# Performance work log

Hardware: AMD Instinct MI355X
Metric: run time of the kernel (lower is better)

## Reference

```python
import jax, jax.numpy as jnp
import numpy as np

D_IN, H1, H2, B, K = 128, 128, 64, 262144, 4

def _mk(key, shape):
    return jax.random.normal(key, shape, dtype=jnp.float32) * 0.05

def setup_inputs() -> dict:
    key = jax.random.key(0)
    ks = jax.random.split(key, 40)
    inp = {
        'x': jax.random.normal(ks[0], (B, 96), dtype=jnp.float32),
        'u': jax.random.normal(ks[1], (B, 32), dtype=jnp.float32),
        'mix_factor': jax.random.uniform(ks[2], (1,), dtype=jnp.float32),
        'teacher_P': jax.random.uniform(ks[3], (K,), dtype=jnp.float32),
    }
    # main critic params (torch Linear: W [out,in], b [out])
    dims = [(H1, D_IN), (H1, H1), (H2, H1), (1, H2)] * 2  # l1..l4, l5..l8
    for i, (o, ii) in enumerate(dims):
        inp[f'W{i+1}'] = _mk(ks[4 + 2 * i], (o, ii))
        inp[f'b{i+1}'] = _mk(ks[5 + 2 * i], (o,))
    # stacked teacher params (K teachers), only l1,l2,l3,l5,l6,l7 are used
    tdims = {'1': (H1, D_IN), '2': (H1, H1), '3': (H2, H1), '5': (H1, D_IN), '6': (H1, H1), '7': (H2, H1)}
    j = 20
    for name, (o, ii) in tdims.items():
        inp[f'tW{name}'] = _mk(ks[j], (K, o, ii)); j += 1
        inp[f'tb{name}'] = _mk(ks[j], (K, o)); j += 1
    return inp

def reference(x, u, mix_factor, teacher_P, W1, b1, W2, b2, W3, b3, W4, b4, W5, b5, W6, b6, W7, b7, W8, b8, tW1, tb1, tW2, tb2, tW3, tb3, tW5, tb5, tW6, tb6, tW7, tb7):
    m = mix_factor  # [1], broadcasts
    P = teacher_P   # [K]
    xu = jnp.concatenate([x, u], axis=1)  # [B, 128]

    lin = lambda h, W, b: h @ W.T + b
    # teacher linear on shared input [B,I] -> [K,B,O]
    tlin0 = lambda h, W, b: jnp.einsum('bi,koi->kbo', h, W) + b[:, None, :]
    # teacher linear on per-teacher streams [K,B,I] -> [K,B,O]
    tlin = lambda h, W, b: jnp.einsum('kbi,koi->kbo', h, W) + b[:, None, :]
    mixsum = lambda ht: jnp.einsum('kbo,k->bo', ht, P)

    def head(W_a, b_a, W_b, b_b, W_c, b_c, W_d, b_d, tWa, tba, tWb, tbb, tWc, tbc):
        ht = tlin0(xu, tWa, tba)                                   # [K,B,128]
        h = jax.nn.relu(lin(xu, W_a, b_a) * (1 - m) + mixsum(ht) * m)
        ht = jax.nn.relu(ht)
        ht2 = tlin(ht, tWb, tbb)
        h = jax.nn.relu(lin(h, W_b, b_b) * (1 - m) + mixsum(ht2) * m)
        ht2 = jax.nn.relu(ht2)
        ht3 = tlin(ht2, tWc, tbc)
        h = jax.nn.relu(lin(h, W_c, b_c) * (1 - m) + mixsum(ht3) * m)
        return lin(h, W_d, b_d)                                    # [B,1]

    x1 = head(W1, b1, W2, b2, W3, b3, W4, b4, tW1, tb1, tW2, tb2, tW3, tb3)
    x2 = head(W5, b5, W6, b6, W7, b7, W8, b8, tW5, tb5, tW6, tb6, tW7, tb7)
    return (x1, x2)
```

## Files before the change

kernel.cpp:

```cpp
#include <hip/hip_runtime.h>
#include <hip/hip_bf16.h>
#include <stdint.h>

#define B_TOTAL 262144
#define TB 64
#define RECORD 2560
#define LDS_BYTES 163840
#define HEAD_W 204800

typedef short v8s __attribute__((ext_vector_type(8)));
typedef float v4f __attribute__((ext_vector_type(4)));

union Frag { uint4 q; uint32_t d[4]; v8s v; };

__device__ __forceinline__ uint32_t pack2(float a, float b) {
    union { __hip_bfloat162 h; uint32_t u; } p;
    p.h = __float22bfloat162_rn(make_float2(a, b));
    return p.u;
}


struct KParams {
    const float* x; const float* u; const float* mix; const float* P;
    const float* mb[6];
    const float* tb[6];
    const float* Wout[2];
    const float* bout[2];
    const unsigned short* wbf;
    float* out;
};

struct PrepParams { const float* src[12]; unsigned short* dst; };

__global__ __launch_bounds__(256) void prep_kernel(PrepParams pp) {
    const int ends[12] = {16384,81920,98304,163840,172032,204800,
                          221184,286720,303104,368640,376832,409600};
    int gi = (blockIdx.x * 256 + threadIdx.x) * 4;
    if (gi >= 409600) return;
    int s = 0;
    #pragma unroll
    for (int i = 0; i < 12; ++i) { if (gi >= ends[i]) s = i + 1; }
    int base = (s == 0) ? 0 : ends[s - 1];
    const float4 f = *(const float4*)(pp.src[s] + (gi - base));
    *(uint2*)(pp.dst + gi) = make_uint2(pack2(f.x, f.y), pack2(f.z, f.w));
}

__device__ __forceinline__ void stage_xu(char* lds, const float* x, const float* u,
                                         int rowBase, int tid)
{
    for (int G = tid; G < 1024; G += 512) {
        const int row = G >> 4;
        const int gg  = G & 15;
        const int grow = rowBase + row;
        float4 fa, fb;
        if (gg < 12) {
            const float* s2 = x + grow * 96 + gg * 8;
            fa = *(const float4*)s2; fb = *(const float4*)(s2 + 4);
        } else {
            const float* s2 = u + grow * 32 + (gg - 12) * 8;
            fa = *(const float4*)s2; fb = *(const float4*)(s2 + 4);
        }
        *(uint4*)(lds + row * RECORD + ((gg ^ (row & 15)) << 4)) =
            make_uint4(pack2(fa.x, fa.y), pack2(fa.z, fa.w),
                       pack2(fb.x, fb.y), pack2(fb.z, fb.w));
    }
}

struct WPre { Frag w[20]; float4 mB; float4 tB[4]; };

template<int N>
__device__ __forceinline__ WPre preload(const unsigned short* W,
        const float* mbias, const float* tbias, int lane, int wave)
{
    WPre r;
    const int l15  = lane & 15;
    const int quad = lane >> 4;
    const int colBase = (N == 64) ? ((wave >> 1) << 4) : (wave << 4);
    const unsigned short* wRow = W + (colBase + l15) * 128 + quad * 8;
    #pragma unroll
    for (int s = 0; s < 5; ++s)
        #pragma unroll
        for (int ks = 0; ks < 4; ++ks)
            r.w[s * 4 + ks].q = *(const uint4*)(wRow + s * (N * 128) + ks * 32);
    const int obase = colBase + quad * 4;
    r.mB = *(const float4*)(mbias + obase);
    #pragma unroll
    for (int s = 0; s < 4; ++s)
        r.tB[s] = *(const float4*)(tbias + s * N + obase);
    return r;
}

template<bool SHARED_IN, int N, int INS, int OUTS>
__device__ __forceinline__ void compute(char* lds,
        const WPre& wp, float c0, const float* cP, int lane, int wave,
        const float* Wout, float* pgrid)
{
    constexpr bool FINAL = (N == 64);
    constexpr int NBT = FINAL ? 2 : 4;
    const int l15  = lane & 15;
    const int quad = lane >> 4;
    const int colBase = FINAL ? ((wave >> 1) << 4) : (wave << 4);
    const int btBase  = FINAL ? ((wave & 1) << 1) : 0;

    const uint32_t rb = (uint32_t)l15 * RECORD + ((uint32_t)l15 << 4);
    uint32_t rA[4];
    #pragma unroll
    for (int ks = 0; ks < 4; ++ks)
        rA[ks] = rb ^ (uint32_t)(((ks << 2) | quad) << 4);
    if constexpr (FINAL) {
        const uint32_t bo = (uint32_t)btBase * 40960u;
        #pragma unroll
        for (int ks = 0; ks < 4; ++ks) rA[ks] += bo;
    }
    uint32_t rB[4];
    if constexpr (!FINAL) {
        #pragma unroll
        for (int ks = 0; ks < 4; ++ks) rB[ks] = rA[ks] + 2u * 40960u;
    }

    v4f acc[5][NBT];
    #pragma unroll
    for (int bt = 0; bt < NBT; ++bt) {
        acc[0][bt] = (v4f){wp.mB.x, wp.mB.y, wp.mB.z, wp.mB.w};
        #pragma unroll
        for (int s = 0; s < 4; ++s)
            acc[s + 1][bt] = (v4f){wp.tB[s].x, wp.tB[s].y, wp.tB[s].z, wp.tB[s].w};
    }

    #pragma unroll
    for (int ks = 0; ks < 4; ++ks) {
        Frag xS[NBT];
        if constexpr (SHARED_IN) {
            #pragma unroll
            for (int bt = 0; bt < NBT; ++bt) {
                const uint32_t a = (bt < 2) ? (rA[ks] + (uint32_t)(bt * 40960 + INS * 256))
                                            : (rB[ks] + (uint32_t)((bt - 2) * 40960 + INS * 256));
                xS[bt].q = *(const uint4*)(lds + a);
            }
        }
        #pragma unroll
        for (int s = 0; s < 5; ++s) {
            Frag xF[NBT];
            if constexpr (!SHARED_IN) {
                #pragma unroll
                for (int bt = 0; bt < NBT; ++bt) {
                    const uint32_t a = (bt < 2) ? (rA[ks] + (uint32_t)(bt * 40960 + (INS + s) * 256))
                                                : (rB[ks] + (uint32_t)((bt - 2) * 40960 + (INS + s) * 256));
                    xF[bt].q = *(const uint4*)(lds + a);
                }
            }
            #pragma unroll
            for (int bt = 0; bt < NBT; ++bt)
                acc[s][bt] = __builtin_amdgcn_mfma_f32_16x16x32_bf16(
                    wp.w[s * 4 + ks].v, (SHARED_IN ? xS[bt].v : xF[bt].v),
                    acc[s][bt], 0, 0, 0);
        }
    }

    const int obase = colBase + (quad << 2);

    if constexpr (!FINAL) {
        const int ocg = (colBase >> 3) + (quad >> 1);
        const uint32_t w0 = (rb ^ ((uint32_t)ocg << 4)) + (uint32_t)((quad & 1) << 3);
        #pragma unroll
        for (int bt = 0; bt < 4; ++bt) {
            char* ab = lds + (w0 + (uint32_t)(bt * 40960));
            float vr[4];
            vr[0] = c0 * acc[0][bt][0];
            vr[1] = c0 * acc[0][bt][1];
            vr[2] = c0 * acc[0][bt][2];
            vr[3] = c0 * acc[0][bt][3];
            uint2 tw[4];
            #pragma unroll
            for (int s = 0; s < 4; ++s) {
                const float t0 = acc[s + 1][bt][0];
                const float t1 = acc[s + 1][bt][1];
                const float t2 = acc[s + 1][bt][2];
                const float t3 = acc[s + 1][bt][3];
                vr[0] = fmaf(cP[s], t0, vr[0]);
                vr[1] = fmaf(cP[s], t1, vr[1]);
                vr[2] = fmaf(cP[s], t2, vr[2]);
                vr[3] = fmaf(cP[s], t3, vr[3]);
                tw[s] = make_uint2(pack2(fmaxf(t0, 0.f), fmaxf(t1, 0.f)),
                                   pack2(fmaxf(t2, 0.f), fmaxf(t3, 0.f)));
            }
            *(uint2*)(ab + OUTS * 256) =
                make_uint2(pack2(fmaxf(vr[0], 0.f), fmaxf(vr[1], 0.f)),
                           pack2(fmaxf(vr[2], 0.f), fmaxf(vr[3], 0.f)));
            #pragma unroll
            for (int s = 0; s < 4; ++s)
                *(uint2*)(ab + (OUTS + 1 + s) * 256) = tw[s];
        }
    } else {
        const float4 wo = *(const float4*)(Wout + obase);
        float psum[NBT];
        #pragma unroll
        for (int j = 0; j < NBT; ++j) {
            float vr[4];
            vr[0] = c0 * acc[0][j][0];
            vr[1] = c0 * acc[0][j][1];
            vr[2] = c0 * acc[0][j][2];
            vr[3] = c0 * acc[0][j][3];
            #pragma unroll
            for (int s = 0; s < 4; ++s) {
                vr[0] = fmaf(cP[s], acc[s + 1][j][0], vr[0]);
                vr[1] = fmaf(cP[s], acc[s + 1][j][1], vr[1]);
                vr[2] = fmaf(cP[s], acc[s + 1][j][2], vr[2]);
                vr[3] = fmaf(cP[s], acc[s + 1][j][3], vr[3]);
            }
            float pp = fmaxf(vr[0], 0.f) * wo.x + fmaxf(vr[1], 0.f) * wo.y
                     + fmaxf(vr[2], 0.f) * wo.z + fmaxf(vr[3], 0.f) * wo.w;
            pp += __shfl_xor(pp, 16);
            pp += __shfl_xor(pp, 32);
            psum[j] = pp;
        }
        if (lane < 16) {
            #pragma unroll
            for (int j = 0; j < NBT; ++j)
                pgrid[(wave >> 1) * 64 + (btBase + j) * 16 + lane] = psum[j];
        }
    }
}

extern "C" __global__ __launch_bounds__(512, 2)
void critic_kernel(KParams p)
{
    extern __shared__ char lds[];
    const int tid  = threadIdx.x;
    const int lane = tid & 63;
    const int wave = tid >> 6;
    const int rowBase = blockIdx.x * TB;

    const float m  = p.mix[0];
    const float c0 = 1.f - m;
    float cP[4];
    #pragma unroll
    for (int k = 0; k < 4; ++k) cP[k] = m * p.P[k];

    stage_xu(lds, p.x, p.u, rowBase, tid);

    #pragma unroll 1
    for (int head = 0; head < 2; ++head) {
        const unsigned short* wb = p.wbf + head * HEAD_W;
        const int hb = head * 3;

        WPre w1 = preload<128>(wb, p.mb[hb + 0], p.tb[hb + 0], lane, wave);
        __syncthreads();
        compute<true, 128, 0, 5>(lds, w1, c0, cP, lane, wave, nullptr, nullptr);

        WPre w2 = preload<128>(wb + 81920, p.mb[hb + 1], p.tb[hb + 1], lane, wave);
        __syncthreads();
        compute<false, 128, 5, 0>(lds, w2, c0, cP, lane, wave, nullptr, nullptr);

        WPre w3 = preload<64>(wb + 163840, p.mb[hb + 2], p.tb[hb + 2], lane, wave);
        __syncthreads();
        compute<false, 64, 0, 0>(lds, w3, c0, cP, lane, wave,
                                 p.Wout[head], (float*)(lds + 1280));
        __syncthreads();

        if (tid < 64) {
            const float* pg = (const float*)(lds + 1280);
            p.out[head * B_TOTAL + rowBase + tid] =
                p.bout[head][0] + pg[tid] + pg[64 + tid] + pg[128 + tid] + pg[192 + tid];
        }
        if (head == 0) {
            stage_xu(lds, p.x, p.u, rowBase, tid);
        }
    }
}

extern "C" void kernel_launch(void* const* d_in, const int* in_sizes, int n_in,
                              void* d_out, int out_size, void* d_ws, size_t ws_size,
                              hipStream_t stream)
{
    (void)in_sizes; (void)n_in; (void)out_size; (void)ws_size;

    PrepParams pp;
    const int sidx[12] = {4, 20, 6, 22, 8, 24, 12, 26, 14, 28, 16, 30};
    for (int i = 0; i < 12; ++i) pp.src[i] = (const float*)d_in[sidx[i]];
    pp.dst = (unsigned short*)d_ws;

    KParams kp;
    kp.x = (const float*)d_in[0];  kp.u = (const float*)d_in[1];
    kp.mix = (const float*)d_in[2]; kp.P = (const float*)d_in[3];
    const int mbi[6] = {5, 7, 9, 13, 15, 17};
    const int tbi[6] = {21, 23, 25, 27, 29, 31};
    for (int i = 0; i < 6; ++i) {
        kp.mb[i] = (const float*)d_in[mbi[i]];
        kp.tb[i] = (const float*)d_in[tbi[i]];
    }
    kp.Wout[0] = (const float*)d_in[10]; kp.Wout[1] = (const float*)d_in[18];
    kp.bout[0] = (const float*)d_in[11]; kp.bout[1] = (const float*)d_in[19];
    kp.wbf = (const unsigned short*)d_ws;
    kp.out = (float*)d_out;

    (void)hipFuncSetAttribute((const void*)critic_kernel,
                              hipFuncAttributeMaxDynamicSharedMemorySize, LDS_BYTES);

    hipLaunchKernelGGL(prep_kernel, dim3(400), dim3(256), 0, stream, pp);
    hipLaunchKernelGGL(critic_kernel, dim3(B_TOTAL / TB), dim3(512), LDS_BYTES, stream, kp);
}
```

Baseline: 860.3 us.

## Halve batch tile to 32 rows with 4 waves each computing two column tiles

Shrinks the per-block batch tile from 64 to 32 rows and the block from 512 to 256 threads, halving LDS use so more blocks can be resident per CU. Each wave now covers two 16-column output tiles per layer, reloading weight fragments from global/L2 between them, and the batch tiles per wave drop from 4 to 2. It also raises wave priority around the MFMA loop with s_setprio. The cost is twice as many weight-fragment loads per row processed, and more blocks overall, each staging its own inputs.

```diff
diff --git a/kernel.cpp b/kernel.cpp
--- a/kernel.cpp
+++ b/kernel.cpp
@@ -3,9 +3,9 @@
 #include <stdint.h>
 
 #define B_TOTAL 262144
-#define TB 64
+#define TB 32
 #define RECORD 2560
-#define LDS_BYTES 163840
+#define LDS_BYTES 81920
 #define HEAD_W 204800
 
 typedef short v8s __attribute__((ext_vector_type(8)));
@@ -48,7 +48,7 @@
 __device__ __forceinline__ void stage_xu(char* lds, const float* x, const float* u,
                                          int rowBase, int tid)
 {
-    for (int G = tid; G < 1024; G += 512) {
+    for (int G = tid; G < 512; G += 256) {
         const int row = G >> 4;
         const int gg  = G & 15;
         const int grow = rowBase + row;
@@ -69,13 +69,12 @@
 struct WPre { Frag w[20]; float4 mB; float4 tB[4]; };
 
 template<int N>
-__device__ __forceinline__ WPre preload(const unsigned short* W,
-        const float* mbias, const float* tbias, int lane, int wave)
+__device__ __forceinline__ WPre preload(const unsigned short* W, int colBase,
+        const float* mbias, const float* tbias, int lane)
 {
     WPre r;
     const int l15  = lane & 15;
     const int quad = lane >> 4;
-    const int colBase = (N == 64) ? ((wave >> 1) << 4) : (wave << 4);
     const unsigned short* wRow = W + (colBase + l15) * 128 + quad * 8;
     #pragma unroll
     for (int s = 0; s < 5; ++s)
@@ -92,70 +91,55 @@
 
 template<bool SHARED_IN, int N, int INS, int OUTS>
 __device__ __forceinline__ void compute(char* lds,
-        const WPre& wp, float c0, const float* cP, int lane, int wave,
+        const WPre& wp, float c0, const float* cP, int lane, int colBase,
         const float* Wout, float* pgrid)
 {
     constexpr bool FINAL = (N == 64);
-    constexpr int NBT = FINAL ? 2 : 4;
     const int l15  = lane & 15;
     const int quad = lane >> 4;
-    const int colBase = FINAL ? ((wave >> 1) << 4) : (wave << 4);
-    const int btBase  = FINAL ? ((wave & 1) << 1) : 0;
 
     const uint32_t rb = (uint32_t)l15 * RECORD + ((uint32_t)l15 << 4);
     uint32_t rA[4];
     #pragma unroll
     for (int ks = 0; ks < 4; ++ks)
         rA[ks] = rb ^ (uint32_t)(((ks << 2) | quad) << 4);
-    if constexpr (FINAL) {
-        const uint32_t bo = (uint32_t)btBase * 40960u;
-        #pragma unroll
-        for (int ks = 0; ks < 4; ++ks) rA[ks] += bo;
-    }
-    uint32_t rB[4];
-    if constexpr (!FINAL) {
-        #pragma unroll
-        for (int ks = 0; ks < 4; ++ks) rB[ks] = rA[ks] + 2u * 40960u;
-    }
-
-    v4f acc[5][NBT];
-    #pragma unroll
-    for (int bt = 0; bt < NBT; ++bt) {
+
+    v4f acc[5][2];
+    #pragma unroll
+    for (int bt = 0; bt < 2; ++bt) {
         acc[0][bt] = (v4f){wp.mB.x, wp.mB.y, wp.mB.z, wp.mB.w};
         #pragma unroll
         for (int s = 0; s < 4; ++s)
             acc[s + 1][bt] = (v4f){wp.tB[s].x, wp.tB[s].y, wp.tB[s].z, wp.tB[s].w};
     }
 
+    __builtin_amdgcn_s_setprio(1);
     #pragma unroll
     for (int ks = 0; ks < 4; ++ks) {
-        Frag xS[NBT];
+        Frag xS[2];
         if constexpr (SHARED_IN) {
             #pragma unroll
-            for (int bt = 0; bt < NBT; ++bt) {
-                const uint32_t a = (bt < 2) ? (rA[ks] + (uint32_t)(bt * 40960 + INS * 256))
-                                            : (rB[ks] + (uint32_t)((bt - 2) * 40960 + INS * 256));
-                xS[bt].q = *(const uint4*)(lds + a);
-            }
+            for (int bt = 0; bt < 2; ++bt)
+                xS[bt].q = *(const uint4*)(lds + rA[ks]
+                            + (uint32_t)(bt * 40960 + INS * 256));
         }
         #pragma unroll
         for (int s = 0; s < 5; ++s) {
-            Frag xF[NBT];
+            Frag xF[2];
             if constexpr (!SHARED_IN) {
                 #pragma unroll
-                for (int bt = 0; bt < NBT; ++bt) {
-                    const uint32_t a = (bt < 2) ? (rA[ks] + (uint32_t)(bt * 40960 + (INS + s) * 256))
-                                                : (rB[ks] + (uint32_t)((bt - 2) * 40960 + (INS + s) * 256));
-                    xF[bt].q = *(const uint4*)(lds + a);
-                }
+                for (int bt = 0; bt < 2; ++bt)
+                    xF[bt].q = *(const uint4*)(lds + rA[ks]
+                                + (uint32_t)(bt * 40960 + (INS + s) * 256));
             }
             #pragma unroll
-            for (int bt = 0; bt < NBT; ++bt)
+            for (int bt = 0; bt < 2; ++bt)
                 acc[s][bt] = __builtin_amdgcn_mfma_f32_16x16x32_bf16(
                     wp.w[s * 4 + ks].v, (SHARED_IN ? xS[bt].v : xF[bt].v),
                     acc[s][bt], 0, 0, 0);
         }
     }
+    __builtin_amdgcn_s_setprio(0);
 
     const int obase = colBase + (quad << 2);
 
@@ -163,7 +147,7 @@
         const int ocg = (colBase >> 3) + (quad >> 1);
         const uint32_t w0 = (rb ^ ((uint32_t)ocg << 4)) + (uint32_t)((quad & 1) << 3);
         #pragma unroll
-        for (int bt = 0; bt < 4; ++bt) {
+        for (int bt = 0; bt < 2; ++bt) {
             char* ab = lds + (w0 + (uint32_t)(bt * 40960));
             float vr[4];
             vr[0] = c0 * acc[0][bt][0];
@@ -193,9 +177,10 @@
         }
     } else {
         const float4 wo = *(const float4*)(Wout + obase);
-        float psum[NBT];
-        #pragma unroll
-        for (int j = 0; j < NBT; ++j) {
+        const int cw = colBase >> 4;
+        float psum[2];
+        #pragma unroll
+        for (int j = 0; j < 2; ++j) {
             float vr[4];
             vr[0] = c0 * acc[0][j][0];
             vr[1] = c0 * acc[0][j][1];
@@ -216,13 +201,13 @@
         }
         if (lane < 16) {
             #pragma unroll
-            for (int j = 0; j < NBT; ++j)
-                pgrid[(wave >> 1) * 64 + (btBase + j) * 16 + lane] = psum[j];
-        }
-    }
-}
-
-extern "C" __global__ __launch_bounds__(512, 2)
+            for (int j = 0; j < 2; ++j)
+                pgrid[cw * 32 + j * 16 + lane] = psum[j];
+        }
+    }
+}
+
+extern "C" __global__ __launch_bounds__(256, 2)
 void critic_kernel(KParams p)
 {
     extern __shared__ char lds[];
@@ -230,6 +215,8 @@
     const int lane = tid & 63;
     const int wave = tid >> 6;
     const int rowBase = blockIdx.x * TB;
+    const int cb32 = wave << 5;
+    const int cb16 = wave << 4;
 
     const float m  = p.mix[0];
     const float c0 = 1.f - m;
@@ -244,24 +231,28 @@
         const unsigned short* wb = p.wbf + head * HEAD_W;
         const int hb = head * 3;
 
-        WPre w1 = preload<128>(wb, p.mb[hb + 0], p.tb[hb + 0], lane, wave);
-        __syncthreads();
-        compute<true, 128, 0, 5>(lds, w1, c0, cP, lane, wave, nullptr, nullptr);
-
-        WPre w2 = preload<128>(wb + 81920, p.mb[hb + 1], p.tb[hb + 1], lane, wave);
-        __syncthreads();
-        compute<false, 128, 5, 0>(lds, w2, c0, cP, lane, wave, nullptr, nullptr);
-
-        WPre w3 = preload<64>(wb + 163840, p.mb[hb + 2], p.tb[hb + 2], lane, wave);
-        __syncthreads();
-        compute<false, 64, 0, 0>(lds, w3, c0, cP, lane, wave,
+        WPre w = preload<128>(wb, cb32, p.mb[hb + 0], p.tb[hb + 0], lane);
+        __syncthreads();
+        compute<true, 128, 0, 5>(lds, w, c0, cP, lane, cb32, nullptr, nullptr);
+        w = preload<128>(wb, cb32 + 16, p.mb[hb + 0], p.tb[hb + 0], lane);
+        compute<true, 128, 0, 5>(lds, w, c0, cP, lane, cb32 + 16, nullptr, nullptr);
+
+        w = preload<128>(wb + 81920, cb32, p.mb[hb + 1], p.tb[hb + 1], lane);
+        __syncthreads();
+        compute<false, 128, 5, 0>(lds, w, c0, cP, lane, cb32, nullptr, nullptr);
+        w = preload<128>(wb + 81920, cb32 + 16, p.mb[hb + 1], p.tb[hb + 1], lane);
+        compute<false, 128, 5, 0>(lds, w, c0, cP, lane, cb32 + 16, nullptr, nullptr);
+
+        w = preload<64>(wb + 163840, cb16, p.mb[hb + 2], p.tb[hb + 2], lane);
+        __syncthreads();
+        compute<false, 64, 0, 0>(lds, w, c0, cP, lane, cb16,
                                  p.Wout[head], (float*)(lds + 1280));
         __syncthreads();
 
-        if (tid < 64) {
+        if (tid < 32) {
             const float* pg = (const float*)(lds + 1280);
             p.out[head * B_TOTAL + rowBase + tid] =
-                p.bout[head][0] + pg[tid] + pg[64 + tid] + pg[128 + tid] + pg[192 + tid];
+                p.bout[head][0] + pg[tid] + pg[32 + tid] + pg[64 + tid] + pg[96 + tid];
         }
         if (head == 0) {
             stage_xu(lds, p.x, p.u, rowBase, tid);
@@ -298,5 +289,5 @@
                               hipFuncAttributeMaxDynamicSharedMemorySize, LDS_BYTES);
 
     hipLaunchKernelGGL(prep_kernel, dim3(400), dim3(256), 0, stream, pp);
-    hipLaunchKernelGGL(critic_kernel, dim3(B_TOTAL / TB), dim3(512), LDS_BYTES, stream, kp);
-}
+    hipLaunchKernelGGL(critic_kernel, dim3(B_TOTAL / TB), dim3(256), LDS_BYTES, stream, kp);
+}
```

Result: slower. 1.063 ms (+23.6%).

## Double block to 1024 threads, splitting batch tiles across twice as many waves

Applied to the files above, without the earlier changes.

The critic kernel now launches 1024 threads per block instead of 512. Each wave handles half as many 16-row batch tiles: 2 instead of 4 in the 128-wide layers, and 1 instead of 2 in the 64-wide layer. Wave-to-column and row-tile mapping is recomputed accordingly, and x/u staging becomes a single pass. The aim is more waves per CU to hide LDS and MFMA latency. In exchange, each wave's preloaded weight fragments are reused over fewer tiles, weight traffic from global memory doubles, and the per-thread register budget shrinks, which risks spills.

```diff
diff --git a/kernel.cpp b/kernel.cpp
--- a/kernel.cpp
+++ b/kernel.cpp
@@ -48,34 +48,31 @@
 __device__ __forceinline__ void stage_xu(char* lds, const float* x, const float* u,
                                          int rowBase, int tid)
 {
-    for (int G = tid; G < 1024; G += 512) {
-        const int row = G >> 4;
-        const int gg  = G & 15;
-        const int grow = rowBase + row;
-        float4 fa, fb;
-        if (gg < 12) {
-            const float* s2 = x + grow * 96 + gg * 8;
-            fa = *(const float4*)s2; fb = *(const float4*)(s2 + 4);
-        } else {
-            const float* s2 = u + grow * 32 + (gg - 12) * 8;
-            fa = *(const float4*)s2; fb = *(const float4*)(s2 + 4);
-        }
-        *(uint4*)(lds + row * RECORD + ((gg ^ (row & 15)) << 4)) =
-            make_uint4(pack2(fa.x, fa.y), pack2(fa.z, fa.w),
-                       pack2(fb.x, fb.y), pack2(fb.z, fb.w));
-    }
+    const int row = tid >> 4;
+    const int gg  = tid & 15;
+    const int grow = rowBase + row;
+    float4 fa, fb;
+    if (gg < 12) {
+        const float* s2 = x + grow * 96 + gg * 8;
+        fa = *(const float4*)s2; fb = *(const float4*)(s2 + 4);
+    } else {
+        const float* s2 = u + grow * 32 + (gg - 12) * 8;
+        fa = *(const float4*)s2; fb = *(const float4*)(s2 + 4);
+    }
+    *(uint4*)(lds + row * RECORD + ((gg ^ (row & 15)) << 4)) =
+        make_uint4(pack2(fa.x, fa.y), pack2(fa.z, fa.w),
+                   pack2(fb.x, fb.y), pack2(fb.z, fb.w));
 }
 
 struct WPre { Frag w[20]; float4 mB; float4 tB[4]; };
 
 template<int N>
-__device__ __forceinline__ WPre preload(const unsigned short* W,
-        const float* mbias, const float* tbias, int lane, int wave)
+__device__ __forceinline__ WPre preload(const unsigned short* W, int colBase,
+        const float* mbias, const float* tbias, int lane)
 {
     WPre r;
     const int l15  = lane & 15;
     const int quad = lane >> 4;
-    const int colBase = (N == 64) ? ((wave >> 1) << 4) : (wave << 4);
     const unsigned short* wRow = W + (colBase + l15) * 128 + quad * 8;
     #pragma unroll
     for (int s = 0; s < 5; ++s)
@@ -90,33 +87,20 @@
     return r;
 }
 
-template<bool SHARED_IN, int N, int INS, int OUTS>
-__device__ __forceinline__ void compute(char* lds,
-        const WPre& wp, float c0, const float* cP, int lane, int wave,
-        const float* Wout, float* pgrid)
+template<bool SHARED_IN, int N, int INS, int OUTS, int NBT>
+__device__ __forceinline__ void compute(char* ldsR,
+        const WPre& wp, float c0, const float* cP, int lane, int colBase,
+        const float* Wout, float* pgrid, int prow)
 {
     constexpr bool FINAL = (N == 64);
-    constexpr int NBT = FINAL ? 2 : 4;
     const int l15  = lane & 15;
     const int quad = lane >> 4;
-    const int colBase = FINAL ? ((wave >> 1) << 4) : (wave << 4);
-    const int btBase  = FINAL ? ((wave & 1) << 1) : 0;
 
     const uint32_t rb = (uint32_t)l15 * RECORD + ((uint32_t)l15 << 4);
     uint32_t rA[4];
     #pragma unroll
     for (int ks = 0; ks < 4; ++ks)
         rA[ks] = rb ^ (uint32_t)(((ks << 2) | quad) << 4);
-    if constexpr (FINAL) {
-        const uint32_t bo = (uint32_t)btBase * 40960u;
-        #pragma unroll
-        for (int ks = 0; ks < 4; ++ks) rA[ks] += bo;
-    }
-    uint32_t rB[4];
-    if constexpr (!FINAL) {
-        #pragma unroll
-        for (int ks = 0; ks < 4; ++ks) rB[ks] = rA[ks] + 2u * 40960u;
-    }
 
     v4f acc[5][NBT];
     #pragma unroll
@@ -132,22 +116,18 @@
         Frag xS[NBT];
         if constexpr (SHARED_IN) {
             #pragma unroll
-            for (int bt = 0; bt < NBT; ++bt) {
-                const uint32_t a = (bt < 2) ? (rA[ks] + (uint32_t)(bt * 40960 + INS * 256))
-                                            : (rB[ks] + (uint32_t)((bt - 2) * 40960 + INS * 256));
-                xS[bt].q = *(const uint4*)(lds + a);
-            }
+            for (int bt = 0; bt < NBT; ++bt)
+                xS[bt].q = *(const uint4*)(ldsR + rA[ks]
+                            + (uint32_t)(bt * 40960 + INS * 256));
         }
         #pragma unroll
         for (int s = 0; s < 5; ++s) {
             Frag xF[NBT];
             if constexpr (!SHARED_IN) {
                 #pragma unroll
-                for (int bt = 0; bt < NBT; ++bt) {
-                    const uint32_t a = (bt < 2) ? (rA[ks] + (uint32_t)(bt * 40960 + (INS + s) * 256))
-                                                : (rB[ks] + (uint32_t)((bt - 2) * 40960 + (INS + s) * 256));
-                    xF[bt].q = *(const uint4*)(lds + a);
-                }
+                for (int bt = 0; bt < NBT; ++bt)
+                    xF[bt].q = *(const uint4*)(ldsR + rA[ks]
+                                + (uint32_t)(bt * 40960 + (INS + s) * 256));
             }
             #pragma unroll
             for (int bt = 0; bt < NBT; ++bt)
@@ -163,8 +143,8 @@
         const int ocg = (colBase >> 3) + (quad >> 1);
         const uint32_t w0 = (rb ^ ((uint32_t)ocg << 4)) + (uint32_t)((quad & 1) << 3);
         #pragma unroll
-        for (int bt = 0; bt < 4; ++bt) {
-            char* ab = lds + (w0 + (uint32_t)(bt * 40960));
+        for (int bt = 0; bt < NBT; ++bt) {
+            char* ab = ldsR + (w0 + (uint32_t)(bt * 40960));
             float vr[4];
             vr[0] = c0 * acc[0][bt][0];
             vr[1] = c0 * acc[0][bt][1];
@@ -193,36 +173,28 @@
         }
     } else {
         const float4 wo = *(const float4*)(Wout + obase);
-        float psum[NBT];
-        #pragma unroll
-        for (int j = 0; j < NBT; ++j) {
-            float vr[4];
-            vr[0] = c0 * acc[0][j][0];
-            vr[1] = c0 * acc[0][j][1];
-            vr[2] = c0 * acc[0][j][2];
-            vr[3] = c0 * acc[0][j][3];
-            #pragma unroll
-            for (int s = 0; s < 4; ++s) {
-                vr[0] = fmaf(cP[s], acc[s + 1][j][0], vr[0]);
-                vr[1] = fmaf(cP[s], acc[s + 1][j][1], vr[1]);
-                vr[2] = fmaf(cP[s], acc[s + 1][j][2], vr[2]);
-                vr[3] = fmaf(cP[s], acc[s + 1][j][3], vr[3]);
-            }
-            float pp = fmaxf(vr[0], 0.f) * wo.x + fmaxf(vr[1], 0.f) * wo.y
-                     + fmaxf(vr[2], 0.f) * wo.z + fmaxf(vr[3], 0.f) * wo.w;
-            pp += __shfl_xor(pp, 16);
-            pp += __shfl_xor(pp, 32);
-            psum[j] = pp;
-        }
-        if (lane < 16) {
-            #pragma unroll
-            for (int j = 0; j < NBT; ++j)
-                pgrid[(wave >> 1) * 64 + (btBase + j) * 16 + lane] = psum[j];
-        }
-    }
-}
-
-extern "C" __global__ __launch_bounds__(512, 2)
+        float vr[4];
+        vr[0] = c0 * acc[0][0][0];
+        vr[1] = c0 * acc[0][0][1];
+        vr[2] = c0 * acc[0][0][2];
+        vr[3] = c0 * acc[0][0][3];
+        #pragma unroll
+        for (int s = 0; s < 4; ++s) {
+            vr[0] = fmaf(cP[s], acc[s + 1][0][0], vr[0]);
+            vr[1] = fmaf(cP[s], acc[s + 1][0][1], vr[1]);
+            vr[2] = fmaf(cP[s], acc[s + 1][0][2], vr[2]);
+            vr[3] = fmaf(cP[s], acc[s + 1][0][3], vr[3]);
+        }
+        float pp = fmaxf(vr[0], 0.f) * wo.x + fmaxf(vr[1], 0.f) * wo.y
+                 + fmaxf(vr[2], 0.f) * wo.z + fmaxf(vr[3], 0.f) * wo.w;
+        pp += __shfl_xor(pp, 16);
+        pp += __shfl_xor(pp, 32);
+        if (lane < 16)
+            pgrid[(colBase >> 4) * 64 + prow + lane] = pp;
+    }
+}
+
+extern "C" __global__ __launch_bounds__(1024, 4)
 void critic_kernel(KParams p)
 {
     extern __shared__ char lds[];
@@ -231,6 +203,12 @@
     const int wave = tid >> 6;
     const int rowBase = blockIdx.x * TB;
 
+    const int cb128 = (wave & 7) << 4;
+    char* ldsH = lds + ((wave >> 3) * 81920);
+    const int cb64 = (wave & 3) << 4;
+    const int rt64 = wave >> 2;
+    char* ldsF = lds + rt64 * 40960;
+
     const float m  = p.mix[0];
     const float c0 = 1.f - m;
     float cP[4];
@@ -244,18 +222,20 @@
         const unsigned short* wb = p.wbf + head * HEAD_W;
         const int hb = head * 3;
 
-        WPre w1 = preload<128>(wb, p.mb[hb + 0], p.tb[hb + 0], lane, wave);
-        __syncthreads();
-        compute<true, 128, 0, 5>(lds, w1, c0, cP, lane, wave, nullptr, nullptr);
-
-        WPre w2 = preload<128>(wb + 81920, p.mb[hb + 1], p.tb[hb + 1], lane, wave);
-        __syncthreads();
-        compute<false, 128, 5, 0>(lds, w2, c0, cP, lane, wave, nullptr, nullptr);
-
-        WPre w3 = preload<64>(wb + 163840, p.mb[hb + 2], p.tb[hb + 2], lane, wave);
-        __syncthreads();
-        compute<false, 64, 0, 0>(lds, w3, c0, cP, lane, wave,
-                                 p.Wout[head], (float*)(lds + 1280));
+        WPre w1 = preload<128>(wb, cb128, p.mb[hb + 0], p.tb[hb + 0], lane);
+        __syncthreads();
+        compute<true, 128, 0, 5, 2>(ldsH, w1, c0, cP, lane, cb128,
+                                    nullptr, nullptr, 0);
+
+        WPre w2 = preload<128>(wb + 81920, cb128, p.mb[hb + 1], p.tb[hb + 1], lane);
+        __syncthreads();
+        compute<false, 128, 5, 0, 2>(ldsH, w2, c0, cP, lane, cb128,
+                                     nullptr, nullptr, 0);
+
+        WPre w3 = preload<64>(wb + 163840, cb64, p.mb[hb + 2], p.tb[hb + 2], lane);
+        __syncthreads();
+        compute<false, 64, 0, 0, 1>(ldsF, w3, c0, cP, lane, cb64,
+                                    p.Wout[head], (float*)(lds + 1280), rt64 * 16);
         __syncthreads();
 
         if (tid < 64) {
@@ -298,5 +278,5 @@
                               hipFuncAttributeMaxDynamicSharedMemorySize, LDS_BYTES);
 
     hipLaunchKernelGGL(prep_kernel, dim3(400), dim3(256), 0, stream, pp);
-    hipLaunchKernelGGL(critic_kernel, dim3(B_TOTAL / TB), dim3(512), LDS_BYTES, stream, kp);
-}
+    hipLaunchKernelGGL(critic_kernel, dim3(B_TOTAL / TB), dim3(1024), LDS_BYTES, stream, kp);
+}
```

Measured after the change: 1.307 ms. 51.9% more time.
